# Optimization experiments

Measured on AMD Instinct MI355X. Metric: run time of the kernel, lower is better.

The kernel has to match this reference:

```python
import jax, jax.numpy as jnp
import numpy as np

IGNORE_INDEX = -100
BETA = 0.1
ALPHA = 1.0  # HFAlignmentLoss default; nll term is zero since compute_nll_loss=False

B, T, H, V = 4, 512, 2048, 32000


def setup_inputs() -> dict:
    key = jax.random.key(0)
    k1, k2, k3, k4, k5 = jax.random.split(key, 5)
    scale = 1.0 / np.sqrt(H)
    return {
        "x": jax.random.normal(k1, (B, T, H), dtype=jnp.float32),
        "ref_x": jax.random.normal(k2, (B, T, H), dtype=jnp.float32),
        "y": jax.random.randint(k3, (B, T), 0, V, dtype=jnp.int64),
        "W": jax.random.normal(k4, (V, H), dtype=jnp.float32) * scale,
        "ref_W": jax.random.normal(k5, (V, H), dtype=jnp.float32) * scale,
    }


def _batch_logps(logits, labels):
    """Average per-token label log-prob over non-ignored tokens (average_log_prob=True).
    logits: (B, T, V) float32; labels: (B, T) int. Returns (B,) float32."""
    mask = labels != IGNORE_INDEX
    safe_labels = jnp.where(mask, labels, 0)
    logps = jax.nn.log_softmax(logits, axis=-1)                       # (B, T, V)
    per_tok = jnp.take_along_axis(logps, safe_labels[..., None], axis=-1)[..., 0]
    maskf = mask.astype(logits.dtype)
    return (per_tok * maskf).sum(-1) / maskf.sum(-1)                  # (B,)


def reference(x, ref_x, y, W, ref_W):
    half = x.shape[0] // 2

    # policy LM head (bias=False) -> logits in fp32 (HF ref casts with .float())
    logits = jnp.einsum("bth,vh->btv", x, W).astype(jnp.float32)
    all_logps = _batch_logps(logits, y)
    policy_chosen_logps = all_logps[:half]
    policy_rejected_logps = all_logps[half:]

    # reference LM head (ref_bias=False)
    ref_logits = jnp.einsum("bth,vh->btv", ref_x, ref_W).astype(jnp.float32)
    ref_all_logps = _batch_logps(ref_logits, y)
    ref_chosen_logps = ref_all_logps[:half]
    ref_rejected_logps = ref_all_logps[half:]

    # SPPO-hard alignment loss
    a = policy_chosen_logps - ref_chosen_logps
    b = policy_rejected_logps - ref_rejected_logps
    chosen_rewards = BETA * a
    rejected_rewards = BETA * b
    losses = (a - 0.5 / BETA) ** 2 + (b + 0.5 / BETA) ** 2

    policy_nll_loss = jnp.float32(0.0)  # compute_nll_loss=False
    loss = policy_nll_loss * ALPHA - losses.mean()
    return loss


if __name__ == "__main__":
    out = reference(**setup_inputs())
    print(out)
```

## Files before the change

kernel.cpp:

```cpp
#include <hip/hip_runtime.h>
#include <hip/hip_bf16.h>
#include <math.h>

#define H 2048
#define V 32000
#define T 512
#define TOK 2048
#define IGN (-100)

#define BM 64
#define BN 64
#define BK 32
#define NCH (V / BN)

typedef unsigned short u16;
typedef __attribute__((ext_vector_type(8))) short short8;
typedef __attribute__((ext_vector_type(4))) float f32x4;

__device__ __forceinline__ u16 f2bf(float f) {
    unsigned int u = __float_as_uint(f);
    u += 0x7fffu + ((u >> 16) & 1u);
    return (u16)(u >> 16);
}

#define GLD16(gp, lp) __builtin_amdgcn_global_load_lds( \
    (const __attribute__((address_space(1))) unsigned int*)(gp), \
    (__attribute__((address_space(3))) unsigned int*)(lp), 16, 0, 0)

__global__ __launch_bounds__(256) void f32_to_bf16(
    const float* __restrict__ src, u16* __restrict__ dst, int n4)
{
    for (int i = blockIdx.x * 256 + threadIdx.x; i < n4; i += gridDim.x * 256) {
        float4 v = ((const float4*)src)[i];
        ushort4 o;
        o.x = f2bf(v.x); o.y = f2bf(v.y); o.z = f2bf(v.z); o.w = f2bf(v.w);
        ((ushort4*)dst)[i] = o;
    }
}

__global__ __launch_bounds__(512, 2) void gemm_bf16(
    const u16* __restrict__ Xb, const u16* __restrict__ Wb,
    float* __restrict__ ms_m, float* __restrict__ ms_s)
{
    __shared__ __align__(16) u16 lds[65536];

    const int tid  = threadIdx.x;
    const int wave = tid >> 6;
    const int lane = tid & 63;
    const int q    = lane >> 4;
    const int rl   = lane & 15;
    const int wm   = wave >> 2;
    const int wn   = wave & 3;

    const int lin = (int)blockIdx.x;
    const int wg  = (lin & 7) * 250 + (lin >> 3);
    const int bx  = wg & 7;
    const int rem = wg >> 3;
    const int by  = rem % 125;
    const int model = rem / 125;

    const size_t tokBase = (size_t)bx * 256;
    const size_t vBase   = (size_t)by * 256;

    const u16* __restrict__ A  = Xb + (size_t)model * (2048ULL * H) + tokBase * H;
    const u16* __restrict__ Bm = Wb + (size_t)model * ((size_t)V * H) + vBase * H;
    const u16* __restrict__ A1p = A  + 128 * H;
    const u16* __restrict__ B1p = Bm + 128 * H;

    const int G0 = wave * 64 + lane;
    const int G1 = G0 + 512;
    const int r0 = G0 >> 3, s0 = (G0 & 7) ^ (r0 & 7);
    const int r1 = G1 >> 3, s1 = (G1 & 7) ^ (r1 & 7);
    const int off0 = r0 * H + s0 * 8;
    const int off1 = r1 * H + s1 * 8;
    const int ldsS0 = wave * 512;
    const int ldsS1 = 4096 + wave * 512;

#define STAGE(gp, hb) do { \
    GLD16((gp) + off0, lds + (hb) + ldsS0); \
    GLD16((gp) + off1, lds + (hb) + ldsS1); \
} while (0)

    const int sB = (q ^ (rl & 7)) << 3;
    int aoff[8], boff[4];
#pragma unroll
    for (int im = 0; im < 8; ++im) aoff[im] = (im * 16 + rl) * 64 + sB;
#pragma unroll
    for (int in = 0; in < 4; ++in) boff[in] = ((wn & 1) * 64 + in * 16 + rl) * 64 + sB;

    const int aB0 = wm * 8192;
    const int aB1 = 32768 + wm * 8192;
    const int bB0 = 16384 + (wn >> 1) * 8192;
    const int bB1 = 49152 + (wn >> 1) * 8192;

    short8 af[4][2], bf[4][2];
    f32x4 acc[8][4];
#pragma unroll
    for (int a = 0; a < 8; ++a)
#pragma unroll
        for (int b = 0; b < 4; ++b) acc[a][b] = (f32x4){0.f, 0.f, 0.f, 0.f};

#define LDA(cb, mh) do { \
    _Pragma("unroll") \
    for (int f = 0; f < 4; ++f) { \
        const int o_ = (cb) + aoff[(mh) * 4 + f]; \
        af[f][0] = *(const short8*)(lds + o_); \
        af[f][1] = *(const short8*)(lds + (o_ ^ 32)); \
    } } while (0)

#define LDB(cb) do { \
    _Pragma("unroll") \
    for (int f = 0; f < 4; ++f) { \
        const int o_ = (cb) + boff[f]; \
        bf[f][0] = *(const short8*)(lds + o_); \
        bf[f][1] = *(const short8*)(lds + (o_ ^ 32)); \
    } } while (0)

#define QUAD(mh, nh) do { \
    _Pragma("unroll") \
    for (int f = 0; f < 4; ++f) \
    _Pragma("unroll") \
    for (int g = 0; g < 2; ++g) { \
        acc[(mh)*4+f][(nh)*2+g] = __builtin_amdgcn_mfma_f32_16x16x32_bf16( \
            af[f][0], bf[(nh)*2+g][0], acc[(mh)*4+f][(nh)*2+g], 0, 0, 0); \
        acc[(mh)*4+f][(nh)*2+g] = __builtin_amdgcn_mfma_f32_16x16x32_bf16( \
            af[f][1], bf[(nh)*2+g][1], acc[(mh)*4+f][(nh)*2+g], 0, 0, 0); \
    } } while (0)

#define SYNC_PRE() do { \
    __builtin_amdgcn_s_barrier(); \
    asm volatile("s_waitcnt lgkmcnt(0)" ::: "memory"); \
    __builtin_amdgcn_s_setprio(1); \
} while (0)

#define SYNC_POST() do { \
    __builtin_amdgcn_s_setprio(0); \
    __builtin_amdgcn_s_barrier(); \
    asm volatile("" ::: "memory"); \
} while (0)

    STAGE(Bm,        16384); STAGE(B1p,       24576);
    STAGE(A,             0); STAGE(A1p,        8192);
    STAGE(Bm + 64,   49152); STAGE(B1p + 64,  57344);
    STAGE(A + 64,    32768);
    asm volatile("s_waitcnt vmcnt(6)" ::: "memory");
    __builtin_amdgcn_s_barrier();
    asm volatile("" ::: "memory");

#pragma unroll 1
    for (int i = 0; i < 15; ++i) {
        const int k1 = i * 128 + 64, k2 = k1 + 64, k3 = k2 + 64;
        LDA(aB0, 0); LDB(bB0);
        STAGE(A1p + k1, 40960);
        SYNC_PRE(); QUAD(0, 0); SYNC_POST();
        STAGE(Bm + k2, 16384);
        SYNC_PRE(); QUAD(0, 1); SYNC_POST();
        LDA(aB0, 1);
        STAGE(B1p + k2, 24576);
        SYNC_PRE(); QUAD(1, 1); SYNC_POST();
        STAGE(A + k2, 0);
        asm volatile("s_waitcnt vmcnt(6)" ::: "memory");
        SYNC_PRE(); QUAD(1, 0); SYNC_POST();
        LDA(aB1, 0); LDB(bB1);
        STAGE(A1p + k2, 8192);
        SYNC_PRE(); QUAD(0, 0); SYNC_POST();
        STAGE(Bm + k3, 49152);
        SYNC_PRE(); QUAD(0, 1); SYNC_POST();
        LDA(aB1, 1);
        STAGE(B1p + k3, 57344);
        SYNC_PRE(); QUAD(1, 1); SYNC_POST();
        STAGE(A + k3, 32768);
        asm volatile("s_waitcnt vmcnt(6)" ::: "memory");
        SYNC_PRE(); QUAD(1, 0); SYNC_POST();
    }

    STAGE(A1p + 31 * 64, 40960);
    asm volatile("s_waitcnt vmcnt(0)" ::: "memory");
    __builtin_amdgcn_s_barrier();
    asm volatile("" ::: "memory");

    LDA(aB0, 0); LDB(bB0); QUAD(0, 0); QUAD(0, 1);
    LDA(aB0, 1);           QUAD(1, 0); QUAD(1, 1);
    LDA(aB1, 0); LDB(bB1); QUAD(0, 0); QUAD(0, 1);
    LDA(aB1, 1);           QUAD(1, 0); QUAD(1, 1);

    const int chunk = by * 4 + wn;
    const size_t rowB = (size_t)model * TOK + tokBase + (size_t)wm * 128;
#pragma unroll
    for (int im = 0; im < 8; ++im) {
#pragma unroll
        for (int i2 = 0; i2 < 4; ++i2) {
            float v0 = acc[im][0][i2], v1 = acc[im][1][i2];
            float v2 = acc[im][2][i2], v3 = acc[im][3][i2];
            float mx = fmaxf(fmaxf(v0, v1), fmaxf(v2, v3));
#pragma unroll
            for (int off = 1; off < 16; off <<= 1)
                mx = fmaxf(mx, __shfl_xor(mx, off));
            float s = __expf(v0 - mx) + __expf(v1 - mx)
                    + __expf(v2 - mx) + __expf(v3 - mx);
#pragma unroll
            for (int off = 1; off < 16; off <<= 1)
                s += __shfl_xor(s, off);
            if (rl == 0) {
                size_t idx = (rowB + im * 16 + q * 4 + i2) * NCH + chunk;
                ms_m[idx] = mx;
                ms_s[idx] = s;
            }
        }
    }
#undef STAGE
#undef LDA
#undef LDB
#undef QUAD
#undef SYNC_PRE
#undef SYNC_POST
}

__global__ __launch_bounds__(256) void gemm_partial(
    const float* __restrict__ X,  const float* __restrict__ Xr,
    const float* __restrict__ Wp, const float* __restrict__ Wr,
    float* __restrict__ ms_m, float* __restrict__ ms_s)
{
    __shared__ float smemF[64 * 65];
    short* smemS = (short*)smemF;
    short* ldsA = smemS;
    short* ldsB = smemS + 64 * 40;

    const int tid     = threadIdx.x;
    const int model   = blockIdx.z;
    const int tokBase = blockIdx.x * BM;
    const int vBase   = blockIdx.y * BN;

    const float* __restrict__ Xp = model ? Xr : X;
    const float* __restrict__ Wm = model ? Wr : Wp;

    const int lane = tid & 63;
    const int wave = tid >> 6;
    const int q    = lane >> 4;
    const int rl   = lane & 15;
    const int m0   = (wave >> 1) * 32;
    const int n0   = (wave & 1) * 32;

    f32x4 acc[2][2];
    for (int a = 0; a < 2; a++)
        for (int b = 0; b < 2; b++)
            acc[a][b] = (f32x4){0.f, 0.f, 0.f, 0.f};

    for (int kk = 0; kk < H / BK; kk++) {
        const int k0 = kk * BK;
        __syncthreads();
        for (int rep = 0; rep < 2; rep++) {
            int i   = tid + rep * 256;
            int row = i >> 3;
            int cf  = (i & 7) * 4;
            const float4 va = *(const float4*)(Xp + (size_t)(tokBase + row) * H + k0 + cf);
            short* pa = ldsA + row * 40 + cf;
            pa[0] = (short)f2bf(va.x); pa[1] = (short)f2bf(va.y);
            pa[2] = (short)f2bf(va.z); pa[3] = (short)f2bf(va.w);
            const float4 vb = *(const float4*)(Wm + (size_t)(vBase + row) * H + k0 + cf);
            short* pb = ldsB + row * 40 + cf;
            pb[0] = (short)f2bf(vb.x); pb[1] = (short)f2bf(vb.y);
            pb[2] = (short)f2bf(vb.z); pb[3] = (short)f2bf(vb.w);
        }
        __syncthreads();

        short8 aF[2], bF[2];
        for (int im = 0; im < 2; im++)
            aF[im] = *(const short8*)(ldsA + (m0 + im * 16 + rl) * 40 + q * 8);
        for (int in = 0; in < 2; in++)
            bF[in] = *(const short8*)(ldsB + (n0 + in * 16 + rl) * 40 + q * 8);

        for (int im = 0; im < 2; im++)
            for (int in = 0; in < 2; in++)
                acc[im][in] = __builtin_amdgcn_mfma_f32_16x16x32_bf16(
                    aF[im], bF[in], acc[im][in], 0, 0, 0);
    }

    __syncthreads();
    for (int im = 0; im < 2; im++)
        for (int in = 0; in < 2; in++)
            for (int i = 0; i < 4; i++)
                smemF[(m0 + im * 16 + q * 4 + i) * 65 + (n0 + in * 16 + rl)] =
                    acc[im][in][i];
    __syncthreads();

    if (tid < 64) {
        const float* rowp = smemF + tid * 65;
        float m = -INFINITY;
        for (int j = 0; j < 64; j++) m = fmaxf(m, rowp[j]);
        float s = 0.f;
        for (int j = 0; j < 64; j++) s += __expf(rowp[j] - m);
        size_t idx = ((size_t)model * TOK + (tokBase + tid)) * NCH + blockIdx.y;
        ms_m[idx] = m;
        ms_s[idx] = s;
    }
}

__global__ __launch_bounds__(256) void label_logit(
    const float* __restrict__ X,  const float* __restrict__ Xr,
    const float* __restrict__ Wp, const float* __restrict__ Wr,
    const int* __restrict__ y, float* __restrict__ z)
{
    int id    = blockIdx.x * 4 + (threadIdx.x >> 6);
    int lane  = threadIdx.x & 63;
    int model = id >> 11;
    int token = id & 2047;
    const float* __restrict__ Xp = model ? Xr : X;
    const float* __restrict__ Wm = model ? Wr : Wp;
    int lab = y[token];
    float sum = 0.f;
    if (lab != IGN) {
        const float* xp = Xp + (size_t)token * H;
        const float* wp = Wm + (size_t)lab * H;
        for (int c = lane; c < H; c += 64) sum += xp[c] * wp[c];
    }
    for (int off = 32; off; off >>= 1) sum += __shfl_down(sum, off);
    if (lane == 0) z[id] = sum;
}

__global__ __launch_bounds__(256) void lse_logp(
    const float* __restrict__ ms_m, const float* __restrict__ ms_s,
    const float* __restrict__ z, float* __restrict__ logp)
{
    int id = blockIdx.x;
    int t  = threadIdx.x;
    __shared__ float red[256];
    const float* mrow = ms_m + (size_t)id * NCH;
    const float* srow = ms_s + (size_t)id * NCH;

    float m = -INFINITY;
    for (int c = t; c < NCH; c += 256) m = fmaxf(m, mrow[c]);
    red[t] = m; __syncthreads();
    for (int w = 128; w; w >>= 1) {
        if (t < w) red[t] = fmaxf(red[t], red[t + w]);
        __syncthreads();
    }
    float M = red[0]; __syncthreads();

    float s = 0.f;
    for (int c = t; c < NCH; c += 256) s += srow[c] * __expf(mrow[c] - M);
    red[t] = s; __syncthreads();
    for (int w = 128; w; w >>= 1) {
        if (t < w) red[t] += red[t + w];
        __syncthreads();
    }
    if (t == 0) {
        float lse = M + logf(red[0]);
        logp[id] = z[id] - lse;
    }
}

__global__ void final_loss(const float* __restrict__ logp,
                           const int* __restrict__ y,
                           float* __restrict__ out)
{
    __shared__ float lp[8];
    int t = threadIdx.x;
    if (t < 8) {
        int model = t >> 2, b = t & 3;
        float s = 0.f, cnt = 0.f;
        for (int i = 0; i < T; i++) {
            int tok = b * T + i;
            if (y[tok] != IGN) { s += logp[model * TOK + tok]; cnt += 1.f; }
        }
        lp[t] = s / cnt;
    }
    __syncthreads();
    if (t == 0) {
        float a0 = lp[0] - lp[4], a1 = lp[1] - lp[5];
        float b0 = lp[2] - lp[6], b1 = lp[3] - lp[7];
        float l0 = (a0 - 5.f) * (a0 - 5.f) + (b0 + 5.f) * (b0 + 5.f);
        float l1 = (a1 - 5.f) * (a1 - 5.f) + (b1 + 5.f) * (b1 + 5.f);
        out[0] = -(l0 + l1) * 0.5f;
    }
}

extern "C" void kernel_launch(void* const* d_in, const int* in_sizes, int n_in,
                              void* d_out, int out_size, void* d_ws, size_t ws_size,
                              hipStream_t stream)
{
    const float* X  = (const float*)d_in[0];
    const float* Xr = (const float*)d_in[1];
    const int*   y  = (const int*)d_in[2];
    const float* Wp = (const float*)d_in[3];
    const float* Wr = (const float*)d_in[4];
    float* out = (float*)d_out;

    float* ws   = (float*)d_ws;
    const size_t msElems = (size_t)2 * TOK * NCH;
    float* ms_m = ws;
    float* ms_s = ws + msElems;
    float* z    = ws + 2 * msElems;
    float* logp = z + 2 * TOK;
    u16*   Xb   = (u16*)(logp + 2 * TOK);
    u16*   Wb   = Xb + (size_t)2 * 2048 * H;

    const size_t NEED = 2 * msElems * 4 + 4 * 2 * TOK * 4
                      + (size_t)2 * 2048 * H * 2 + (size_t)2 * V * H * 2;

    if (ws_size >= NEED) {
        f32_to_bf16<<<1024, 256, 0, stream>>>(X,  Xb,                 (2048 * H) / 4);
        f32_to_bf16<<<1024, 256, 0, stream>>>(Xr, Xb + 2048 * H,      (2048 * H) / 4);
        f32_to_bf16<<<4096, 256, 0, stream>>>(Wp, Wb,                 (V * H) / 4);
        f32_to_bf16<<<4096, 256, 0, stream>>>(Wr, Wb + (size_t)V * H, (V * H) / 4);

        dim3 gg(2000);
        gemm_bf16<<<gg, 512, 0, stream>>>(Xb, Wb, ms_m, ms_s);
    } else {
        dim3 g1(TOK / BM, V / BN, 2);
        gemm_partial<<<g1, 256, 0, stream>>>(X, Xr, Wp, Wr, ms_m, ms_s);
    }

    label_logit<<<(2 * TOK) / 4, 256, 0, stream>>>(X, Xr, Wp, Wr, y, z);
    lse_logp<<<2 * TOK, 256, 0, stream>>>(ms_m, ms_s, z, logp);
    final_loss<<<1, 64, 0, stream>>>(logp, y, out);
}
```

Baseline: 1.142 ms.

## Re-tile waves to 4x2 and software-pipeline LDS fragment loads across MFMA quads

Changes the wave layout from 2x4 to 4x2 so each wave computes 64 rows by 128 columns, and splits B fragments into per-quad loads that are prefetched while the previous quad's MFMAs run. Barrier and waitcnt placement is restructured so LDS reads for the next quad overlap compute, with partial lgkmcnt waits. The peeled epilogue is folded into the main loop using clamped k offsets. This aims to hide LDS latency and reduce stalls, at the cost of redundant final-iteration loads and more delicate synchronization ordering.

```diff
diff --git a/kernel.cpp b/kernel.cpp
--- a/kernel.cpp
+++ b/kernel.cpp
@@ -49,8 +49,10 @@
     const int lane = tid & 63;
     const int q    = lane >> 4;
     const int rl   = lane & 15;
-    const int wm   = wave >> 2;
-    const int wn   = wave & 3;
+    const int wm   = wave >> 1;
+    const int wn   = wave & 1;
+    const int ah   = wm >> 1;
+    const int am   = wm & 1;
 
     const int lin = (int)blockIdx.x;
     const int wg  = (lin & 7) * 250 + (lin >> 3);
@@ -62,8 +64,8 @@
     const size_t tokBase = (size_t)bx * 256;
     const size_t vBase   = (size_t)by * 256;
 
-    const u16* __restrict__ A  = Xb + (size_t)model * (2048ULL * H) + tokBase * H;
-    const u16* __restrict__ Bm = Wb + (size_t)model * ((size_t)V * H) + vBase * H;
+    const u16* __restrict__ A   = Xb + (size_t)model * (2048ULL * H) + tokBase * H;
+    const u16* __restrict__ Bm  = Wb + (size_t)model * ((size_t)V * H) + vBase * H;
     const u16* __restrict__ A1p = A  + 128 * H;
     const u16* __restrict__ B1p = Bm + 128 * H;
 
@@ -82,138 +84,152 @@
 } while (0)
 
     const int sB = (q ^ (rl & 7)) << 3;
-    int aoff[8], boff[4];
-#pragma unroll
-    for (int im = 0; im < 8; ++im) aoff[im] = (im * 16 + rl) * 64 + sB;
-#pragma unroll
-    for (int in = 0; in < 4; ++in) boff[in] = ((wn & 1) * 64 + in * 16 + rl) * 64 + sB;
-
-    const int aB0 = wm * 8192;
-    const int aB1 = 32768 + wm * 8192;
-    const int bB0 = 16384 + (wn >> 1) * 8192;
-    const int bB1 = 49152 + (wn >> 1) * 8192;
-
-    short8 af[4][2], bf[4][2];
-    f32x4 acc[8][4];
-#pragma unroll
-    for (int a = 0; a < 8; ++a)
-#pragma unroll
-        for (int b = 0; b < 4; ++b) acc[a][b] = (f32x4){0.f, 0.f, 0.f, 0.f};
-
-#define LDA(cb, mh) do { \
+    int aoff[4], pb[2];
+#pragma unroll
+    for (int f = 0; f < 4; ++f) aoff[f] = (am * 64 + f * 16 + rl) * 64 + sB;
+#pragma unroll
+    for (int fn = 0; fn < 2; ++fn) pb[fn] = (fn * 16 + rl) * 64 + sB;
+
+    short8 af[4][2];
+    short8 bf[2][2][2];
+    f32x4 acc[4][8];
+#pragma unroll
+    for (int a = 0; a < 4; ++a)
+#pragma unroll
+        for (int b = 0; b < 8; ++b) acc[a][b] = (f32x4){0.f, 0.f, 0.f, 0.f};
+
+#define LDA(buf) do { \
     _Pragma("unroll") \
     for (int f = 0; f < 4; ++f) { \
-        const int o_ = (cb) + aoff[(mh) * 4 + f]; \
+        const int o_ = (buf) * 32768 + ah * 8192 + aoff[f]; \
         af[f][0] = *(const short8*)(lds + o_); \
         af[f][1] = *(const short8*)(lds + (o_ ^ 32)); \
     } } while (0)
 
-#define LDB(cb) do { \
+#define LDBQ(buf, Q) do { \
     _Pragma("unroll") \
-    for (int f = 0; f < 4; ++f) { \
-        const int o_ = (cb) + boff[f]; \
-        bf[f][0] = *(const short8*)(lds + o_); \
-        bf[f][1] = *(const short8*)(lds + (o_ ^ 32)); \
+    for (int fn = 0; fn < 2; ++fn) { \
+        const int o_ = 16384 + (buf) * 32768 + wn * 8192 + (Q) * 2048 + pb[fn]; \
+        bf[(Q) & 1][fn][0] = *(const short8*)(lds + o_); \
+        bf[(Q) & 1][fn][1] = *(const short8*)(lds + (o_ ^ 32)); \
     } } while (0)
 
-#define QUAD(mh, nh) do { \
+#define QUAD(Q) do { \
+    __builtin_amdgcn_s_setprio(1); \
+    _Pragma("unroll") \
+    for (int ks = 0; ks < 2; ++ks) \
     _Pragma("unroll") \
     for (int f = 0; f < 4; ++f) \
     _Pragma("unroll") \
-    for (int g = 0; g < 2; ++g) { \
-        acc[(mh)*4+f][(nh)*2+g] = __builtin_amdgcn_mfma_f32_16x16x32_bf16( \
-            af[f][0], bf[(nh)*2+g][0], acc[(mh)*4+f][(nh)*2+g], 0, 0, 0); \
-        acc[(mh)*4+f][(nh)*2+g] = __builtin_amdgcn_mfma_f32_16x16x32_bf16( \
-            af[f][1], bf[(nh)*2+g][1], acc[(mh)*4+f][(nh)*2+g], 0, 0, 0); \
-    } } while (0)
-
-#define SYNC_PRE() do { \
-    __builtin_amdgcn_s_barrier(); \
-    asm volatile("s_waitcnt lgkmcnt(0)" ::: "memory"); \
-    __builtin_amdgcn_s_setprio(1); \
+    for (int fn = 0; fn < 2; ++fn) \
+        acc[f][(Q) * 2 + fn] = __builtin_amdgcn_mfma_f32_16x16x32_bf16( \
+            af[f][ks], bf[(Q) & 1][fn][ks], acc[f][(Q) * 2 + fn], 0, 0, 0); \
+    __builtin_amdgcn_s_setprio(0); \
 } while (0)
 
-#define SYNC_POST() do { \
-    __builtin_amdgcn_s_setprio(0); \
-    __builtin_amdgcn_s_barrier(); \
-    asm volatile("" ::: "memory"); \
-} while (0)
-
-    STAGE(Bm,        16384); STAGE(B1p,       24576);
-    STAGE(A,             0); STAGE(A1p,        8192);
-    STAGE(Bm + 64,   49152); STAGE(B1p + 64,  57344);
-    STAGE(A + 64,    32768);
-    asm volatile("s_waitcnt vmcnt(6)" ::: "memory");
+#define PREBAR()  do { __builtin_amdgcn_s_barrier(); asm volatile("" ::: "memory"); } while (0)
+#define POST0()   do { asm volatile("s_waitcnt lgkmcnt(0)" ::: "memory"); \
+                       __builtin_amdgcn_s_barrier(); asm volatile("" ::: "memory"); } while (0)
+#define POST8()   do { asm volatile("s_waitcnt lgkmcnt(8)" ::: "memory"); \
+                       __builtin_amdgcn_s_barrier(); asm volatile("" ::: "memory"); } while (0)
+#define VMCNT(n)  asm volatile("s_waitcnt vmcnt(" #n ")" ::: "memory")
+
+    STAGE(Bm,       16384); STAGE(B1p,      24576);
+    STAGE(A,            0); STAGE(A1p,       8192);
+    STAGE(Bm + 64,  49152);
+    VMCNT(2);
     __builtin_amdgcn_s_barrier();
     asm volatile("" ::: "memory");
+    LDA(0);
+    LDBQ(0, 0);
 
 #pragma unroll 1
-    for (int i = 0; i < 15; ++i) {
-        const int k1 = i * 128 + 64, k2 = k1 + 64, k3 = k2 + 64;
-        LDA(aB0, 0); LDB(bB0);
+    for (int i = 0; i < 16; ++i) {
+        const int u  = 2 * i;
+        const int k1 = (u + 1) * 64;
+        const int k2 = (u + 2 < 32 ? u + 2 : 31) * 64;
+        const int k3 = (u + 3 < 32 ? u + 3 : 31) * 64;
+        LDBQ(0, 1);
+        STAGE(B1p + k1, 57344);
+        PREBAR(); QUAD(0); POST0();
+        LDBQ(0, 2);
+        STAGE(A + k1, 32768);
+        PREBAR(); QUAD(1); POST0();
+        LDBQ(0, 3);
         STAGE(A1p + k1, 40960);
-        SYNC_PRE(); QUAD(0, 0); SYNC_POST();
+        PREBAR(); QUAD(2);
+        VMCNT(4); POST0();
+        LDBQ(1, 0);
         STAGE(Bm + k2, 16384);
-        SYNC_PRE(); QUAD(0, 1); SYNC_POST();
-        LDA(aB0, 1);
+        VMCNT(2); PREBAR();
+        QUAD(3);
+        LDA(1);
+        POST8();
+        LDBQ(1, 1);
         STAGE(B1p + k2, 24576);
-        SYNC_PRE(); QUAD(1, 1); SYNC_POST();
+        PREBAR(); QUAD(0); POST0();
+        LDBQ(1, 2);
         STAGE(A + k2, 0);
-        asm volatile("s_waitcnt vmcnt(6)" ::: "memory");
-        SYNC_PRE(); QUAD(1, 0); SYNC_POST();
-        LDA(aB1, 0); LDB(bB1);
+        PREBAR(); QUAD(1); POST0();
+        LDBQ(1, 3);
         STAGE(A1p + k2, 8192);
-        SYNC_PRE(); QUAD(0, 0); SYNC_POST();
+        PREBAR(); QUAD(2);
+        VMCNT(4); POST0();
+        LDBQ(0, 0);
         STAGE(Bm + k3, 49152);
-        SYNC_PRE(); QUAD(0, 1); SYNC_POST();
-        LDA(aB1, 1);
-        STAGE(B1p + k3, 57344);
-        SYNC_PRE(); QUAD(1, 1); SYNC_POST();
-        STAGE(A + k3, 32768);
-        asm volatile("s_waitcnt vmcnt(6)" ::: "memory");
-        SYNC_PRE(); QUAD(1, 0); SYNC_POST();
-    }
-
-    STAGE(A1p + 31 * 64, 40960);
-    asm volatile("s_waitcnt vmcnt(0)" ::: "memory");
-    __builtin_amdgcn_s_barrier();
-    asm volatile("" ::: "memory");
-
-    LDA(aB0, 0); LDB(bB0); QUAD(0, 0); QUAD(0, 1);
-    LDA(aB0, 1);           QUAD(1, 0); QUAD(1, 1);
-    LDA(aB1, 0); LDB(bB1); QUAD(0, 0); QUAD(0, 1);
-    LDA(aB1, 1);           QUAD(1, 0); QUAD(1, 1);
-
-    const int chunk = by * 4 + wn;
-    const size_t rowB = (size_t)model * TOK + tokBase + (size_t)wm * 128;
-#pragma unroll
-    for (int im = 0; im < 8; ++im) {
+        VMCNT(2); PREBAR();
+        QUAD(3);
+        LDA(0);
+        POST8();
+    }
+
+    const int cA = by * 4 + wn * 2;
+    const size_t rowB = (size_t)model * TOK + tokBase + (size_t)wm * 64;
+#pragma unroll
+    for (int f = 0; f < 4; ++f) {
 #pragma unroll
         for (int i2 = 0; i2 < 4; ++i2) {
-            float v0 = acc[im][0][i2], v1 = acc[im][1][i2];
-            float v2 = acc[im][2][i2], v3 = acc[im][3][i2];
-            float mx = fmaxf(fmaxf(v0, v1), fmaxf(v2, v3));
+            float a0 = acc[f][0][i2], a1 = acc[f][1][i2];
+            float a2 = acc[f][2][i2], a3 = acc[f][3][i2];
+            float mA = fmaxf(fmaxf(a0, a1), fmaxf(a2, a3));
 #pragma unroll
             for (int off = 1; off < 16; off <<= 1)
-                mx = fmaxf(mx, __shfl_xor(mx, off));
-            float s = __expf(v0 - mx) + __expf(v1 - mx)
-                    + __expf(v2 - mx) + __expf(v3 - mx);
+                mA = fmaxf(mA, __shfl_xor(mA, off));
+            float sA = __expf(a0 - mA) + __expf(a1 - mA)
+                     + __expf(a2 - mA) + __expf(a3 - mA);
 #pragma unroll
             for (int off = 1; off < 16; off <<= 1)
-                s += __shfl_xor(s, off);
+                sA += __shfl_xor(sA, off);
+
+            float b0 = acc[f][4][i2], b1 = acc[f][5][i2];
+            float b2 = acc[f][6][i2], b3 = acc[f][7][i2];
+            float mB = fmaxf(fmaxf(b0, b1), fmaxf(b2, b3));
+#pragma unroll
+            for (int off = 1; off < 16; off <<= 1)
+                mB = fmaxf(mB, __shfl_xor(mB, off));
+            float sB2 = __expf(b0 - mB) + __expf(b1 - mB)
+                      + __expf(b2 - mB) + __expf(b3 - mB);
+#pragma unroll
+            for (int off = 1; off < 16; off <<= 1)
+                sB2 += __shfl_xor(sB2, off);
+
             if (rl == 0) {
-                size_t idx = (rowB + im * 16 + q * 4 + i2) * NCH + chunk;
-                ms_m[idx] = mx;
-                ms_s[idx] = s;
+                size_t idx = (rowB + f * 16 + q * 4 + i2) * NCH + cA;
+                ms_m[idx]     = mA;
+                ms_s[idx]     = sA;
+                ms_m[idx + 1] = mB;
+                ms_s[idx + 1] = sB2;
             }
         }
     }
 #undef STAGE
 #undef LDA
-#undef LDB
+#undef LDBQ
 #undef QUAD
-#undef SYNC_PRE
-#undef SYNC_POST
+#undef PREBAR
+#undef POST0
+#undef POST8
+#undef VMCNT
 }
 
 __global__ __launch_bounds__(256) void gemm_partial(
```

Measured after the change: 1.103 ms. 3.4% less time.
